# Kernel optimization log

Measured on AMD Instinct MI355X. Metric: run time of the kernel, lower is better.

The kernel has to match this reference:

```python
import jax, jax.numpy as jnp
import numpy as np

GROUP = 32  # quantization group size along K, fixed by the call site


def setup_inputs() -> dict:
    key = jax.random.key(0)
    k1, k2, k3 = jax.random.split(key, 3)
    M, K, N = 1, 8192, 16384
    A = jax.random.normal(k1, (M, K), dtype=jnp.float16)
    # packed int4 weights: each byte holds two nibbles -> [N, K//2]
    B = jax.random.randint(k2, (N, K // 2), 0, 256, dtype=jnp.int32)
    scalesAndZeros = (jax.random.normal(k3, (N, K // GROUP, 2), dtype=jnp.float16))
    return {"A": A, "B": B, "scalesAndZeros": scalesAndZeros}


def _dequant(B, scalesAndZeros):
    # B: [N, K//2] bytes, two int4 values per byte (low nibble = even k)
    N, Kh = B.shape
    K = Kh * 2
    low = B & 0xF
    high = (B >> 4) & 0xF
    q = jnp.stack([low, high], axis=-1).reshape(N, K).astype(jnp.float32) - 8.0
    scales = scalesAndZeros[..., 0].astype(jnp.float32)  # [N, K//GROUP]
    zeros = scalesAndZeros[..., 1].astype(jnp.float32)   # [N, K//GROUP]
    qg = q.reshape(N, K // GROUP, GROUP)
    W = qg * scales[:, :, None] + zeros[:, :, None]       # [N, K//GROUP, GROUP]
    return W.reshape(N, K)


def reference(A, B, scalesAndZeros):
    # int4 weight-only quantized GEMV: out[m, n] = sum_k A[m, k] * dequant(W)[n, k]
    W = _dequant(B, scalesAndZeros)                        # [N, K] fp32
    out = jnp.einsum("mk,nk->mn", A.astype(jnp.float32), W)
    return out.astype(A.dtype)                             # [1, N] fp16
```

## Files before the change

### kernel.cpp

```cpp
#include <hip/hip_runtime.h>
#include <hip/hip_bf16.h>


#define ROWS 8
#define TPB  512

typedef int ivec4 __attribute__((ext_vector_type(4)));

__global__ __launch_bounds__(TPB, 4) void gemv_w4nt(
    const float4* __restrict__ A4,
    const ivec4*  __restrict__ B,
    const float2* __restrict__ SZ,
    float* __restrict__ out,
    int N)
{
    const int t  = threadIdx.x;
    const int n0 = blockIdx.x * ROWS;

    __shared__ float2 sz_s[ROWS * 256];
    __shared__ float  red[ROWS][8];

    float a[2][8];
    float sAj[2];
#pragma unroll
    for (int j = 0; j < 2; ++j) {
        const int i = t + 512 * j;
        const float4 x = A4[2 * i];
        const float4 y = A4[2 * i + 1];
        a[j][0] = x.x; a[j][1] = x.y; a[j][2] = x.z; a[j][3] = x.w;
        a[j][4] = y.x; a[j][5] = y.y; a[j][6] = y.z; a[j][7] = y.w;
        sAj[j] = ((x.x + x.y) + (x.z + x.w)) + ((y.x + y.y) + (y.z + y.w));
    }

    {
        const float2* Sp = SZ + (size_t)n0 * 256;
#pragma unroll
        for (int q = 0; q < 4; ++q) {
            const int idx = t + TPB * q;
            sz_s[idx] = Sp[idx];
        }
    }
    __syncthreads();

    const ivec4* Bp = B + (size_t)n0 * 1024 + t;
    ivec4 b[ROWS][2];
#pragma unroll
    for (int r = 0; r < ROWS; ++r) {
#pragma unroll
        for (int j = 0; j < 2; ++j)
            b[r][j] = __builtin_nontemporal_load(&Bp[1024 * r + 512 * j]);
    }

    const int g0 = t >> 2;
    float acc[ROWS];
#pragma unroll
    for (int r = 0; r < ROWS; ++r) acc[r] = 0.0f;

#pragma unroll
    for (int r = 0; r < ROWS; ++r) {
#pragma unroll
        for (int j = 0; j < 2; ++j) {
            const float2 sz = sz_s[r * 256 + g0 + 128 * j];
            const int bb[4] = { b[r][j][0], b[r][j][1], b[r][j][2], b[r][j][3] };
            float dot = 0.0f;
#pragma unroll
            for (int m = 0; m < 4; ++m) {
                dot = fmaf(a[j][2 * m],     (float)(bb[m] & 0xF),        dot);
                dot = fmaf(a[j][2 * m + 1], (float)((bb[m] >> 4) & 0xF), dot);
            }
            const float s  = sz.x;
            const float zz = fmaf(-8.0f, s, sz.y);
            acc[r] = fmaf(s, dot, acc[r]);
            acc[r] = fmaf(zz, sAj[j], acc[r]);
        }
    }

    const int lane = t & 63;
    const int w    = t >> 6;
#pragma unroll
    for (int r = 0; r < ROWS; ++r) {
        float v = acc[r];
#pragma unroll
        for (int off = 32; off > 0; off >>= 1)
            v += __shfl_down(v, off, 64);
        if (lane == 0) red[r][w] = v;
    }
    __syncthreads();
    if (t < ROWS) {
        const int n = n0 + t;
        if (n < N) {
            float v = 0.0f;
#pragma unroll
            for (int w2 = 0; w2 < 8; ++w2) v += red[t][w2];
            out[n] = v;
        }
    }
}

extern "C" void kernel_launch(void* const* d_in, const int* in_sizes, int n_in,
                              void* d_out, int out_size, void* d_ws, size_t ws_size,
                              hipStream_t stream) {
    const float4* A4 = (const float4*)d_in[0];
    const ivec4*  B  = (const ivec4*)d_in[1];
    const float2* SZ = (const float2*)d_in[2];
    float* out = (float*)d_out;

    const int N = out_size;
    gemv_w4nt<<<N / ROWS, TPB, 0, stream>>>(A4, B, SZ, out, N);
}
```

Measured before the change: 357.0 us.

## Shrink blocks to two rows, drop shared scale staging, load scales directly

Each block now handles 2 rows with 256 threads instead of 8 rows with 512, giving many more blocks and a higher occupancy hint. The shared-memory staging of scales/zeros and its barrier are removed; each thread reads its scale pair straight from global memory with nontemporal loads. The activation vector is loaded per pass rather than all at once. This aims to improve latency hiding and drop a sync, at the cost of more reloads of A across blocks and more scattered scale loads.

After: 382.5 us. +7.1%, slower.

```diff
diff --git a/kernel.cpp b/kernel.cpp
--- a/kernel.cpp
+++ b/kernel.cpp
@@ -1,80 +1,67 @@
 #include <hip/hip_runtime.h>
-#include <hip/hip_bf16.h>
 
 
-#define ROWS 8
-#define TPB  512
+#define ROWS   2
+#define TPB    256
+#define PASSES 4
 
-typedef int ivec4 __attribute__((ext_vector_type(4)));
+typedef int   ivec4 __attribute__((ext_vector_type(4)));
+typedef float fvec2 __attribute__((ext_vector_type(2)));
 
-__global__ __launch_bounds__(TPB, 4) void gemv_w4nt(
+__global__ __launch_bounds__(TPB, 8) void gemv_w4hi(
     const float4* __restrict__ A4,
     const ivec4*  __restrict__ B,
-    const float2* __restrict__ SZ,
+    const fvec2*  __restrict__ SZ,
     float* __restrict__ out,
     int N)
 {
     const int t  = threadIdx.x;
     const int n0 = blockIdx.x * ROWS;
 
-    __shared__ float2 sz_s[ROWS * 256];
-    __shared__ float  red[ROWS][8];
+    const ivec4* B0 = B + (size_t)n0 * 1024 + t;
+    ivec4 b[PASSES][ROWS];
+#pragma unroll
+    for (int p = 0; p < PASSES; ++p)
+#pragma unroll
+        for (int r = 0; r < ROWS; ++r)
+            b[p][r] = __builtin_nontemporal_load(&B0[(size_t)r * 1024 + p * 256]);
 
-    float a[2][8];
-    float sAj[2];
-#pragma unroll
-    for (int j = 0; j < 2; ++j) {
-        const int i = t + 512 * j;
-        const float4 x = A4[2 * i];
-        const float4 y = A4[2 * i + 1];
-        a[j][0] = x.x; a[j][1] = x.y; a[j][2] = x.z; a[j][3] = x.w;
-        a[j][4] = y.x; a[j][5] = y.y; a[j][6] = y.z; a[j][7] = y.w;
-        sAj[j] = ((x.x + x.y) + (x.z + x.w)) + ((y.x + y.y) + (y.z + y.w));
-    }
-
-    {
-        const float2* Sp = SZ + (size_t)n0 * 256;
-#pragma unroll
-        for (int q = 0; q < 4; ++q) {
-            const int idx = t + TPB * q;
-            sz_s[idx] = Sp[idx];
-        }
-    }
-    __syncthreads();
-
-    const ivec4* Bp = B + (size_t)n0 * 1024 + t;
-    ivec4 b[ROWS][2];
-#pragma unroll
-    for (int r = 0; r < ROWS; ++r) {
-#pragma unroll
-        for (int j = 0; j < 2; ++j)
-            b[r][j] = __builtin_nontemporal_load(&Bp[1024 * r + 512 * j]);
-    }
-
-    const int g0 = t >> 2;
     float acc[ROWS];
 #pragma unroll
     for (int r = 0; r < ROWS; ++r) acc[r] = 0.0f;
 
 #pragma unroll
-    for (int r = 0; r < ROWS; ++r) {
+    for (int p = 0; p < PASSES; ++p) {
+        const int i = t + 256 * p;
+        const float4 x = A4[2 * i];
+        const float4 y = A4[2 * i + 1];
+        const float a0 = x.x, a1 = x.y, a2 = x.z, a3 = x.w;
+        const float a4 = y.x, a5 = y.y, a6 = y.z, a7 = y.w;
+        const float sA = ((a0 + a1) + (a2 + a3)) + ((a4 + a5) + (a6 + a7));
+        const int g = i >> 2;
 #pragma unroll
-        for (int j = 0; j < 2; ++j) {
-            const float2 sz = sz_s[r * 256 + g0 + 128 * j];
-            const int bb[4] = { b[r][j][0], b[r][j][1], b[r][j][2], b[r][j][3] };
+        for (int r = 0; r < ROWS; ++r) {
+            const fvec2 sz =
+                __builtin_nontemporal_load(&SZ[(size_t)(n0 + r) * 256 + g]);
+            const int b0 = b[p][r][0], b1 = b[p][r][1];
+            const int b2 = b[p][r][2], b3 = b[p][r][3];
             float dot = 0.0f;
-#pragma unroll
-            for (int m = 0; m < 4; ++m) {
-                dot = fmaf(a[j][2 * m],     (float)(bb[m] & 0xF),        dot);
-                dot = fmaf(a[j][2 * m + 1], (float)((bb[m] >> 4) & 0xF), dot);
-            }
-            const float s  = sz.x;
-            const float zz = fmaf(-8.0f, s, sz.y);
-            acc[r] = fmaf(s, dot, acc[r]);
-            acc[r] = fmaf(zz, sAj[j], acc[r]);
+            dot = fmaf(a0, (float)(b0 & 0xF),        dot);
+            dot = fmaf(a1, (float)((b0 >> 4) & 0xF), dot);
+            dot = fmaf(a2, (float)(b1 & 0xF),        dot);
+            dot = fmaf(a3, (float)((b1 >> 4) & 0xF), dot);
+            dot = fmaf(a4, (float)(b2 & 0xF),        dot);
+            dot = fmaf(a5, (float)((b2 >> 4) & 0xF), dot);
+            dot = fmaf(a6, (float)(b3 & 0xF),        dot);
+            dot = fmaf(a7, (float)((b3 >> 4) & 0xF), dot);
+            const float s  = sz[0];
+            const float zz = fmaf(-8.0f, s, sz[1]);
+            acc[r] = fmaf(s,  dot, acc[r]);
+            acc[r] = fmaf(zz, sA,  acc[r]);
         }
     }
 
+    __shared__ float red[ROWS][TPB / 64];
     const int lane = t & 63;
     const int w    = t >> 6;
 #pragma unroll
@@ -91,7 +78,7 @@
         if (n < N) {
             float v = 0.0f;
 #pragma unroll
-            for (int w2 = 0; w2 < 8; ++w2) v += red[t][w2];
+            for (int w2 = 0; w2 < TPB / 64; ++w2) v += red[t][w2];
             out[n] = v;
         }
     }
@@ -102,9 +89,9 @@
                               hipStream_t stream) {
     const float4* A4 = (const float4*)d_in[0];
     const ivec4*  B  = (const ivec4*)d_in[1];
-    const float2* SZ = (const float2*)d_in[2];
+    const fvec2*  SZ = (const fvec2*)d_in[2];
     float* out = (float*)d_out;
 
     const int N = out_size;
-    gemv_w4nt<<<N / ROWS, TPB, 0, stream>>>(A4, B, SZ, out, N);
+    gemv_w4hi<<<N / ROWS, TPB, 0, stream>>>(A4, B, SZ, out, N);
 }
```

## Software-pipeline GEMV over row tiles with double-buffered weight loads

Applied to the files above, without the earlier changes.

Each block now handles 32 rows in 16 tiles of 2 rows, prefetching the next tile's packed weights and scales into registers while computing the current tile. Shared-memory scale buffers and reduction slots are double-buffered. The aim is to hide global load latency within a block instead of relying on many short-lived blocks. The trade-off is fewer blocks (512 instead of 2048), which lowers parallelism, plus a barrier per tile.

Measured after the change: 351.5 us. About the same (-1.5%).

```diff
diff --git a/kernel.cpp b/kernel.cpp
--- a/kernel.cpp
+++ b/kernel.cpp
@@ -1,27 +1,30 @@
 #include <hip/hip_runtime.h>
-#include <hip/hip_bf16.h>
 
 
-#define ROWS 8
-#define TPB  512
+#define TPB   512
+#define ROWS  2
+#define TILES 16
+#define CROWS (ROWS * TILES)
 
-typedef int ivec4 __attribute__((ext_vector_type(4)));
+typedef int   ivec4 __attribute__((ext_vector_type(4)));
+typedef float fvec2 __attribute__((ext_vector_type(2)));
 
-__global__ __launch_bounds__(TPB, 4) void gemv_w4nt(
+__global__ __launch_bounds__(TPB, 4) void gemv_w4pipe(
     const float4* __restrict__ A4,
     const ivec4*  __restrict__ B,
-    const float2* __restrict__ SZ,
+    const fvec2*  __restrict__ SZ,
     float* __restrict__ out,
     int N)
 {
-    const int t  = threadIdx.x;
-    const int n0 = blockIdx.x * ROWS;
+    const int t    = threadIdx.x;
+    const int row0 = blockIdx.x * CROWS;
+    const int g0   = t >> 2;
 
-    __shared__ float2 sz_s[ROWS * 256];
-    __shared__ float  red[ROWS][8];
+    __shared__ fvec2 sz_s[2][ROWS * 256];
+    __shared__ float red[2][ROWS][TPB / 64];
 
     float a[2][8];
-    float sAj[2];
+    float sA[2];
 #pragma unroll
     for (int j = 0; j < 2; ++j) {
         const int i = t + 512 * j;
@@ -29,71 +32,88 @@
         const float4 y = A4[2 * i + 1];
         a[j][0] = x.x; a[j][1] = x.y; a[j][2] = x.z; a[j][3] = x.w;
         a[j][4] = y.x; a[j][5] = y.y; a[j][6] = y.z; a[j][7] = y.w;
-        sAj[j] = ((x.x + x.y) + (x.z + x.w)) + ((y.x + y.y) + (y.z + y.w));
+        sA[j] = ((x.x + x.y) + (x.z + x.w)) + ((y.x + y.y) + (y.z + y.w));
     }
 
-    {
-        const float2* Sp = SZ + (size_t)n0 * 256;
+    ivec4 bufA[ROWS][2], bufB[ROWS][2];
+    fvec2 szrA, szrB;
+
+    auto issue = [&](int T, ivec4 (&buf)[ROWS][2], fvec2& szr) {
+        const int rt = row0 + T * ROWS;
+        szr = __builtin_nontemporal_load(&SZ[(size_t)rt * 256 + t]);
+        const ivec4* Bp = B + (size_t)rt * 1024 + t;
 #pragma unroll
-        for (int q = 0; q < 4; ++q) {
-            const int idx = t + TPB * q;
-            sz_s[idx] = Sp[idx];
+        for (int r = 0; r < ROWS; ++r)
+#pragma unroll
+            for (int j = 0; j < 2; ++j)
+                buf[r][j] = __builtin_nontemporal_load(&Bp[r * 1024 + 512 * j]);
+    };
+
+    auto consume = [&](const ivec4 (&buf)[ROWS][2], const fvec2* szl,
+                       float (&redb)[ROWS][TPB / 64]) {
+        float acc[ROWS];
+#pragma unroll
+        for (int r = 0; r < ROWS; ++r) acc[r] = 0.0f;
+#pragma unroll
+        for (int r = 0; r < ROWS; ++r) {
+#pragma unroll
+            for (int j = 0; j < 2; ++j) {
+                const fvec2 sz = szl[r * 256 + g0 + 128 * j];
+                const int b0 = buf[r][j][0], b1 = buf[r][j][1];
+                const int b2 = buf[r][j][2], b3 = buf[r][j][3];
+                float dot = 0.0f;
+                dot = fmaf(a[j][0], (float)(b0 & 0xF),        dot);
+                dot = fmaf(a[j][1], (float)((b0 >> 4) & 0xF), dot);
+                dot = fmaf(a[j][2], (float)(b1 & 0xF),        dot);
+                dot = fmaf(a[j][3], (float)((b1 >> 4) & 0xF), dot);
+                dot = fmaf(a[j][4], (float)(b2 & 0xF),        dot);
+                dot = fmaf(a[j][5], (float)((b2 >> 4) & 0xF), dot);
+                dot = fmaf(a[j][6], (float)(b3 & 0xF),        dot);
+                dot = fmaf(a[j][7], (float)((b3 >> 4) & 0xF), dot);
+                acc[r] = fmaf(sz[0], dot, acc[r]);
+                acc[r] = fmaf(fmaf(-8.0f, sz[0], sz[1]), sA[j], acc[r]);
+            }
         }
-    }
+        const int lane = t & 63;
+        const int w    = t >> 6;
+#pragma unroll
+        for (int r = 0; r < ROWS; ++r) {
+            float v = acc[r];
+#pragma unroll
+            for (int off = 32; off > 0; off >>= 1)
+                v += __shfl_down(v, off, 64);
+            if (lane == 0) redb[r][w] = v;
+        }
+    };
+
+    auto store2 = [&](int T, const float (&redb)[ROWS][TPB / 64]) {
+        if (t < ROWS) {
+            const int n = row0 + T * ROWS + t;
+            if (n < N) {
+                float v = 0.0f;
+#pragma unroll
+                for (int w2 = 0; w2 < TPB / 64; ++w2) v += redb[t][w2];
+                out[n] = v;
+            }
+        }
+    };
+
+    issue(0, bufA, szrA);
+    sz_s[0][t] = szrA;
     __syncthreads();
 
-    const ivec4* Bp = B + (size_t)n0 * 1024 + t;
-    ivec4 b[ROWS][2];
-#pragma unroll
-    for (int r = 0; r < ROWS; ++r) {
-#pragma unroll
-        for (int j = 0; j < 2; ++j)
-            b[r][j] = __builtin_nontemporal_load(&Bp[1024 * r + 512 * j]);
-    }
+    for (int TT = 0; TT < TILES; TT += 2) {
+        if (TT + 1 < TILES) issue(TT + 1, bufB, szrB);
+        consume(bufA, &sz_s[0][0], red[0]);
+        if (TT + 1 < TILES) sz_s[1][t] = szrB;
+        __syncthreads();
+        store2(TT, red[0]);
 
-    const int g0 = t >> 2;
-    float acc[ROWS];
-#pragma unroll
-    for (int r = 0; r < ROWS; ++r) acc[r] = 0.0f;
-
-#pragma unroll
-    for (int r = 0; r < ROWS; ++r) {
-#pragma unroll
-        for (int j = 0; j < 2; ++j) {
-            const float2 sz = sz_s[r * 256 + g0 + 128 * j];
-            const int bb[4] = { b[r][j][0], b[r][j][1], b[r][j][2], b[r][j][3] };
-            float dot = 0.0f;
-#pragma unroll
-            for (int m = 0; m < 4; ++m) {
-                dot = fmaf(a[j][2 * m],     (float)(bb[m] & 0xF),        dot);
-                dot = fmaf(a[j][2 * m + 1], (float)((bb[m] >> 4) & 0xF), dot);
-            }
-            const float s  = sz.x;
-            const float zz = fmaf(-8.0f, s, sz.y);
-            acc[r] = fmaf(s, dot, acc[r]);
-            acc[r] = fmaf(zz, sAj[j], acc[r]);
-        }
-    }
-
-    const int lane = t & 63;
-    const int w    = t >> 6;
-#pragma unroll
-    for (int r = 0; r < ROWS; ++r) {
-        float v = acc[r];
-#pragma unroll
-        for (int off = 32; off > 0; off >>= 1)
-            v += __shfl_down(v, off, 64);
-        if (lane == 0) red[r][w] = v;
-    }
-    __syncthreads();
-    if (t < ROWS) {
-        const int n = n0 + t;
-        if (n < N) {
-            float v = 0.0f;
-#pragma unroll
-            for (int w2 = 0; w2 < 8; ++w2) v += red[t][w2];
-            out[n] = v;
-        }
+        if (TT + 2 < TILES) issue(TT + 2, bufA, szrA);
+        consume(bufB, &sz_s[1][0], red[1]);
+        if (TT + 2 < TILES) sz_s[0][t] = szrA;
+        __syncthreads();
+        store2(TT + 1, red[1]);
     }
 }
 
@@ -102,9 +122,9 @@
                               hipStream_t stream) {
     const float4* A4 = (const float4*)d_in[0];
     const ivec4*  B  = (const ivec4*)d_in[1];
-    const float2* SZ = (const float2*)d_in[2];
+    const fvec2*  SZ = (const fvec2*)d_in[2];
     float* out = (float*)d_out;
 
     const int N = out_size;
-    gemv_w4nt<<<N / ROWS, TPB, 0, stream>>>(A4, B, SZ, out, N);
+    gemv_w4pipe<<<N / CROWS, TPB, 0, stream>>>(A4, B, SZ, out, N);
 }
```
